# Kernel tuning notes

Hardware: AMD Instinct MI355X
Metric: run time of the kernel (lower is better)

## Reference

```python
import jax, jax.numpy as jnp
import numpy as np

N, K, SD, ID, ZD, ED, H, FC, AT, FT = 10000, 31, 8, 2, 32, 64, 128, 128, 16, 6
DT = 0.25


def setup_inputs() -> dict:
    key = jax.random.key(0)
    ks = iter(jax.random.split(key, 48))

    def p(shape, s=0.08):
        return (s * jax.random.normal(next(ks), shape)).astype(jnp.float32)

    E = N * K
    inp = {
        'state_history': p([4, N, SD], 1.0),          # only last slice is used
        'z': p([N, ZD], 1.0),                         # latent code per node
        'edge_idx1': jnp.repeat(jnp.arange(N), K),    # owning node of each edge
        'edge_idx2': jax.random.randint(next(ks), [E], 0, N),  # neighbor node
        'node_obs_idx': 1 + jnp.arange(E).reshape(N, K),  # +1: row 0 of enc table is the zero-pad row
        'W_edge': p([2 * SD, ED]), 'b_edge': jnp.zeros([ED], jnp.float32),
        'att_W1': p([ED, AT]), 'att_W2': p([SD, AT]), 'att_v': p([AT]),
        'obs_Wi': p([ED, 4 * H]), 'obs_Wh': p([H, 4 * H]), 'obs_b': jnp.zeros([4 * H], jnp.float32),
        'st_Wi': p([SD + ID, 4 * H]), 'st_Wh': p([H, 4 * H]), 'st_b': jnp.zeros([4 * H], jnp.float32),
        'oh0_W': p([SD, H]), 'oh0_b': jnp.zeros([H], jnp.float32),
        'oc0_W': p([SD, H]), 'oc0_b': jnp.zeros([H], jnp.float32),
        'sh0_W': p([SD, H]), 'sh0_b': jnp.zeros([H], jnp.float32),
        'sc0_W': p([SD, H]), 'sc0_b': jnp.zeros([H], jnp.float32),
        'act_W1': p([SD + H + H + ZD, FC]), 'act_b1': jnp.zeros([FC], jnp.float32),
        'act_W2': p([FC, ID]), 'act_b2': jnp.zeros([ID], jnp.float32),
        'dyn_A': p([SD, SD]), 'dyn_B': p([SD, ID]),
        'ft': FT,
    }
    return inp


def _lstm_step(x, h, c, Wi, Wh, b):
    g = x @ Wi + h @ Wh + b
    i, f, gg, o = jnp.split(g, 4, axis=-1)  # torch gate order i,f,g,o
    c2 = jax.nn.sigmoid(f) * c + jax.nn.sigmoid(i) * jnp.tanh(gg)
    h2 = jax.nn.sigmoid(o) * jnp.tanh(c2)
    return h2, c2


def reference(state_history, z, edge_idx1, edge_idx2, node_obs_idx,
              W_edge, b_edge, att_W1, att_W2, att_v,
              obs_Wi, obs_Wh, obs_b, st_Wi, st_Wh, st_b,
              oh0_W, oh0_b, oc0_W, oc0_b, sh0_W, sh0_b, sc0_W, sc0_b,
              act_W1, act_b1, act_W2, act_b2, dyn_A, dyn_B, ft):
    s0 = state_history[-1]                      # [N, SD]
    oh = s0 @ oh0_W + oh0_b                     # LSTM initial states from last history state
    oc = s0 @ oc0_W + oc0_b
    sh = s0 @ sh0_W + sh0_b
    sc = s0 @ sc0_W + sc0_b
    u0 = jnp.zeros((s0.shape[0], dyn_B.shape[1]), s0.dtype)

    def step(carry, _):
        s, u, oh, oc, sh, sc = carry
        # heterogeneous edge encoding: gather endpoint states, encode
        e = jnp.concatenate([s[edge_idx1], s[edge_idx2]], axis=-1)   # [E, 2*SD]
        enc = jax.nn.relu(e @ W_edge + b_edge)                       # [E, ED]
        enc_pad = jnp.concatenate([jnp.zeros((1, enc.shape[1]), enc.dtype), enc], axis=0)
        obs = enc_pad[node_obs_idx]                                  # [N, K, ED] gather
        rel = s - s0                                                  # rel_state_fun
        # additive attention over each node's K observed edges
        score = jnp.einsum('nki,i->nk', jnp.tanh(obs @ att_W1 + (rel @ att_W2)[:, None, :]), att_v)
        alpha = jax.nn.softmax(score, axis=-1)
        ctx = jnp.einsum('nk,nke->ne', alpha, obs)                   # [N, ED]
        oh2, oc2 = _lstm_step(ctx, oh, oc, obs_Wi, obs_Wh, obs_b)
        sh2, sc2 = _lstm_step(jnp.concatenate([rel, u], axis=-1), sh, sc, st_Wi, st_Wh, st_b)
        a = jnp.concatenate([rel, oh2, sh2, z], axis=-1)             # [N, SD+2H+ZD]
        u2 = jax.nn.relu(a @ act_W1 + act_b1) @ act_W2 + act_b2      # action net (input_scale=1)
        s2 = s + DT * (s @ dyn_A.T + u2 @ dyn_B.T)                   # dyn_net rollout
        return (s2, u2, oh2, oc2, sh2, sc2), (s2, u2)

    _, (state_pred, input_pred) = jax.lax.scan(step, (s0, u0, oh, oc, sh, sc), None, length=ft)
    return state_pred, input_pred  # [ft, N, SD], [ft, N, ID]
```

## Files before the change

### kernel.cpp

```cpp
#include <hip/hip_runtime.h>
#include <hip/hip_bf16.h>
#include <math.h>

#define N_NODES 10000
#define KE 31
#define SD 8
#define ID 2
#define ZD 32
#define ED 64
#define HH 128
#define FC 128
#define AT 16
#define FT 6
#define DT_C 0.25f
#define NB 4

#define NTU 32
#define MT 2

#define NKS_O 6
#define NKS_S 5
#define NKS_A 10

#define WP_OBS_SZ 49152
#define WP_ST_SZ  40960
#define WP_ACT_SZ 20480
#define WP_EDGE_SZ 1024
#define WP_ATT1_SZ 512

typedef __bf16 bf16x8 __attribute__((ext_vector_type(8)));
typedef float  f32x4  __attribute__((ext_vector_type(4)));

__device__ __forceinline__ float sigm(float x){ return 1.0f/(1.0f+exp2f(-1.44269504f*x)); }
__device__ __forceinline__ float tanh_f(float x){ return 1.0f - 2.0f/(1.0f+exp2f(2.88539008f*x)); }

__device__ __forceinline__ unsigned short f2b(float f){
  __hip_bfloat16 h = __float2bfloat16(f);
  return __builtin_bit_cast(unsigned short, h);
}
__device__ __forceinline__ float b2f(unsigned short x){
  unsigned int u = ((unsigned int)x) << 16;
  return __builtin_bit_cast(float, u);
}
__device__ __forceinline__ unsigned int pack2(float a, float b){
  return (unsigned int)f2b(a) | ((unsigned int)f2b(b) << 16);
}
__device__ __forceinline__ bf16x8 as_bf16x8(int4 v){
  union { int4 i; bf16x8 b; } u; u.i = v; return u.b;
}
__device__ __forceinline__ int hwaddr(int e, int d){
  return e*64 + ((((d>>3)<<3) ^ ((e&7)<<3)) + (d&7));
}

__global__ __launch_bounds__(256) void pack_weights(
    const float* __restrict__ obs_Wi, const float* __restrict__ obs_Wh,
    const float* __restrict__ st_Wi,  const float* __restrict__ st_Wh,
    const float* __restrict__ act_W1, const float* __restrict__ W_edge,
    const float* __restrict__ att_W1,
    unsigned int* __restrict__ wp_obs, unsigned int* __restrict__ wp_st,
    unsigned int* __restrict__ wp_act, unsigned int* __restrict__ wp_edge,
    unsigned int* __restrict__ wp_att1)
{
  int t = blockIdx.x*256 + threadIdx.x;
  if (t < 49152){
    int c = t / 1536; int r = t - c*1536;
    int ks = r >> 8; int q = r & 255;
    int ln = q >> 2; int dw = q & 3;
    int k  = ks*32 + ((ln>>4)<<3) + dw*2;
    int col = (c<<4) + (ln & 15);
    float v0 = (k   < 64) ? obs_Wi[k*4*HH + col]      : obs_Wh[(k-64)*4*HH + col];
    float v1 = (k+1 < 64) ? obs_Wi[(k+1)*4*HH + col]  : obs_Wh[(k-63)*4*HH + col];
    wp_obs[t] = pack2(v0, v1);
  } else if (t < 90112){
    int t2 = t - 49152;
    int c = t2 / 1280; int r = t2 - c*1280;
    int ks = r >> 8; int q = r & 255;
    int ln = q >> 2; int dw = q & 3;
    int k  = ks*32 + ((ln>>4)<<3) + dw*2;
    int col = (c<<4) + (ln & 15);
    float v0, v1;
    { int kk=k;   v0 = (kk<10)? st_Wi[kk*4*HH+col] : (kk<138 ? st_Wh[(kk-10)*4*HH+col] : 0.f); }
    { int kk=k+1; v1 = (kk<10)? st_Wi[kk*4*HH+col] : (kk<138 ? st_Wh[(kk-10)*4*HH+col] : 0.f); }
    wp_st[t2] = pack2(v0, v1);
  } else if (t < 110592){
    int t3 = t - 90112;
    int c = t3 / 2560; int r = t3 - c*2560;
    int ks = r >> 8; int q = r & 255;
    int ln = q >> 2; int dw = q & 3;
    int k  = ks*32 + ((ln>>4)<<3) + dw*2;
    int col = (c<<4) + (ln & 15);
    float v0 = (k   < 296) ? act_W1[k*FC + col]     : 0.f;
    float v1 = (k+1 < 296) ? act_W1[(k+1)*FC + col] : 0.f;
    wp_act[t3] = pack2(v0, v1);
  } else if (t < 111616){
    int t4 = t - 110592;
    int c = t4 >> 8; int r = t4 & 255;
    int ln = r >> 2; int dw = r & 3;
    int k  = ((ln>>4)<<3) + dw*2;
    int col = (c<<4) + (ln & 15);
    float v0 = (k   < 16) ? W_edge[k*ED + col]     : 0.f;
    float v1 = (k+1 < 16) ? W_edge[(k+1)*ED + col] : 0.f;
    wp_edge[t4] = pack2(v0, v1);
  } else if (t < 112128){
    int t5 = t - 111616;
    int ks = t5 >> 8; int r = t5 & 255;
    int ln = r >> 2; int dw = r & 3;
    int k  = ks*32 + ((ln>>4)<<3) + dw*2;
    int col = ln & 15;
    float v0 = (k   < 64) ? att_W1[k*AT + col]     : 0.f;
    float v1 = (k+1 < 64) ? att_W1[(k+1)*AT + col] : 0.f;
    wp_att1[t5] = pack2(v0, v1);
  }
}

__global__ __launch_bounds__(256) void init_kernel(
    const float* __restrict__ s0,
    const float* __restrict__ oh0_W, const float* __restrict__ oh0_b,
    const float* __restrict__ oc0_W, const float* __restrict__ oc0_b,
    const float* __restrict__ sh0_W, const float* __restrict__ sh0_b,
    const float* __restrict__ sc0_W, const float* __restrict__ sc0_b,
    unsigned short* __restrict__ oh, unsigned short* __restrict__ oc,
    unsigned short* __restrict__ sh, unsigned short* __restrict__ sc,
    float* __restrict__ u, unsigned short* __restrict__ s0bf)
{
  int t = blockIdx.x*256 + threadIdx.x;
  if (t < N_NODES*ID) u[t] = 0.0f;
  if (t < N_NODES*SD) s0bf[t] = f2b(s0[t]);
  if (t >= N_NODES*HH) return;
  int n = t >> 7, j = t & 127;
  float s[SD];
  #pragma unroll
  for (int i=0;i<SD;i++) s[i] = s0[n*SD+i];
  float a0=oh0_b[j], a1=oc0_b[j], a2=sh0_b[j], a3=sc0_b[j];
  #pragma unroll
  for (int i=0;i<SD;i++){
    a0 = fmaf(s[i], oh0_W[i*HH+j], a0);
    a1 = fmaf(s[i], oc0_W[i*HH+j], a1);
    a2 = fmaf(s[i], sh0_W[i*HH+j], a2);
    a3 = fmaf(s[i], sc0_W[i*HH+j], a3);
  }
  oh[t]=f2b(a0); oc[t]=f2b(a1); sh[t]=f2b(a2); sc[t]=f2b(a3);
}

__global__ __launch_bounds__(256) void edge_att_mfma(
    const float* __restrict__ s_prev, const float* __restrict__ s0,
    const unsigned short* __restrict__ sprev_bf,
    const int* __restrict__ edge_idx1, const int* __restrict__ edge_idx2,
    const int* __restrict__ node_obs_idx,
    const unsigned int* __restrict__ wp_edge, const unsigned int* __restrict__ wp_att1,
    const float* __restrict__ b_edge, const float* __restrict__ att_W2,
    const float* __restrict__ att_v, unsigned short* __restrict__ ctx)
{
  __shared__ __align__(16) unsigned int eF[8*64*4];
  __shared__ __align__(16) unsigned short encL[128*64];
  __shared__ __align__(16) unsigned int pF[4*64*4];
  __shared__ float scores[128];
  __shared__ float relbuf[NB][SD];
  __shared__ float relW2b[NB][AT];
  __shared__ unsigned char emask[128];

  const int tid  = threadIdx.x;
  const int lane = tid & 63;
  const int w    = tid >> 6;
  const int n0   = blockIdx.x * NB;
  const int EPB  = NB*KE;

  {
    ((uint4*)pF)[tid] = (uint4){0,0,0,0};
    int eb  = tid >> 1;
    int khi = tid & 1;
    int valid = 0;
    uint4 d = (uint4){0,0,0,0};
    if (eb < EPB){
      int nl = eb / KE;
      int j  = eb - nl*KE;
      int idx = node_obs_idx[(n0+nl)*KE + j];
      if (idx > 0){
        valid = 1;
        int e = idx - 1;
        int i = khi ? edge_idx2[e] : edge_idx1[e];
        d = *(const uint4*)&sprev_bf[i*SD];
      }
    }
    int mt = eb >> 4;
    int base = ((mt<<6) + (eb&15) + (khi<<4)) << 2;
    ((uint4*)&eF[base])[0] = d;
    int zbase = ((mt<<6) + (eb&15) + ((khi+2)<<4)) << 2;
    ((uint4*)&eF[zbase])[0] = (uint4){0,0,0,0};
    if (khi == 0) emask[eb] = (unsigned char)valid;
    if (tid < NB*SD){
      int m = tid >> 3, i = tid & 7;
      relbuf[m][i] = s_prev[(n0+m)*SD + i] - s0[(n0+m)*SD + i];
    }
  }
  __syncthreads();

  if (tid < NB*AT){
    int m = tid >> 4, a = tid & 15;
    float acc = 0.f;
    #pragma unroll
    for (int i = 0; i < SD; ++i) acc = fmaf(relbuf[m][i], att_W2[i*AT + a], acc);
    relW2b[m][a] = acc;
  }
  {
    const int c = lane & 15, g = lane >> 4;
    #pragma unroll
    for (int q = 0; q < 2; ++q){
      int mt = w*2 + q;
      bf16x8 A = as_bf16x8(*(const int4*)&eF[((mt<<6) + lane) << 2]);
      f32x4 acc[4];
      #pragma unroll
      for (int ct = 0; ct < 4; ++ct){
        bf16x8 B = as_bf16x8(*(const int4*)&wp_edge[((ct<<6) + lane) << 2]);
        acc[ct] = (f32x4){0,0,0,0};
        acc[ct] = __builtin_amdgcn_mfma_f32_16x16x32_bf16(A, B, acc[ct], 0, 0, 0);
      }
      #pragma unroll
      for (int ct = 0; ct < 4; ++ct){
        int d = ct*16 + c;
        float bias = b_edge[d];
        #pragma unroll
        for (int r = 0; r < 4; ++r){
          int eb = mt*16 + g*4 + r;
          float v = acc[ct][r] + bias;
          v = emask[eb] ? fmaxf(v, 0.f) : 0.f;
          encL[hwaddr(eb, d)] = f2b(v);
        }
      }
    }
  }
  __syncthreads();

  {
    const int c = lane & 15, g = lane >> 4;
    const float av = att_v[c];
    #pragma unroll
    for (int q = 0; q < 2; ++q){
      int mt = w*2 + q;
      int row = mt*16 + c;
      f32x4 acc = (f32x4){0,0,0,0};
      #pragma unroll
      for (int ks = 0; ks < 2; ++ks){
        int hw = row*64 + (((ks*4 + g) << 3) ^ ((row&7) << 3));
        bf16x8 A = *(const bf16x8*)&encL[hw];
        bf16x8 B = as_bf16x8(*(const int4*)&wp_att1[((ks<<6) + lane) << 2]);
        acc = __builtin_amdgcn_mfma_f32_16x16x32_bf16(A, B, acc, 0, 0, 0);
      }
      #pragma unroll
      for (int r = 0; r < 4; ++r){
        int eb = mt*16 + g*4 + r;
        int nm = eb / KE; if (nm > NB-1) nm = NB-1;
        float sv = av * tanh_f(acc[r] + relW2b[nm][c]);
        #pragma unroll
        for (int off = 1; off < 16; off <<= 1) sv += __shfl_xor(sv, off);
        if (c == 0 && eb < EPB) scores[eb] = sv;
      }
    }
  }
  __syncthreads();

  {
    int m = w;
    float sc_ = (lane < KE) ? scores[m*KE + lane] : -INFINITY;
    float mx = sc_;
    #pragma unroll
    for (int off = 32; off; off >>= 1) mx = fmaxf(mx, __shfl_xor(mx, off));
    float p = (lane < KE) ? exp2f(1.44269504f*(sc_ - mx)) : 0.f;
    float sm = p;
    #pragma unroll
    for (int off = 32; off; off >>= 1) sm += __shfl_xor(sm, off);
    float alpha = p / sm;
    if (lane < KE){
      int k = m*KE + lane;
      int ks = k >> 5;
      int ln = m | (((k>>3)&3) << 4);
      ((unsigned short*)pF)[((ks<<6) + ln)*8 + (k&7)] = f2b(alpha);
    }
  }
  __syncthreads();

  {
    const int c = lane & 15, g = lane >> 4;
    const int d = w*16 + c;
    f32x4 acc = (f32x4){0,0,0,0};
    #pragma unroll
    for (int ks = 0; ks < 4; ++ks){
      bf16x8 A = as_bf16x8(*(const int4*)&pF[((ks<<6) + lane) << 2]);
      union { unsigned short u[8]; bf16x8 v; } bb;
      #pragma unroll
      for (int j = 0; j < 8; ++j){
        int e = ks*32 + g*8 + j;
        bb.u[j] = encL[hwaddr(e, d)];
      }
      acc = __builtin_amdgcn_mfma_f32_16x16x32_bf16(A, bb.v, acc, 0, 0, 0);
    }
    if (g == 0){
      #pragma unroll
      for (int r = 0; r < 4; ++r){
        ctx[(n0 + r)*ED + d] = f2b(acc[r]);
      }
    }
  }
}

__global__ __launch_bounds__(1024) void node_update_mfma(
    const float* __restrict__ s_prev, const float* __restrict__ s0,
    const float* __restrict__ z, const unsigned short* __restrict__ ctx,
    const unsigned int* __restrict__ wp_obs, const unsigned int* __restrict__ wp_st,
    const unsigned int* __restrict__ wp_act,
    const float* __restrict__ obs_b, const float* __restrict__ st_b,
    const float* __restrict__ act_b1,
    const float* __restrict__ act_W2, const float* __restrict__ act_b2,
    const float* __restrict__ dyn_A, const float* __restrict__ dyn_B,
    unsigned short* __restrict__ oh, unsigned short* __restrict__ oc,
    unsigned short* __restrict__ sh, unsigned short* __restrict__ sc,
    float* __restrict__ u, float* __restrict__ s_next,
    unsigned short* __restrict__ snext_bf,
    float* __restrict__ out_state, float* __restrict__ out_input, int tstep)
{
  __shared__ __align__(16) union UB {
    struct { unsigned int X1[MT*NKS_O*64*4]; unsigned int X2[MT*NKS_S*64*4]; } x;
    float F[32][FC+4];
  } ubuf;
  __shared__ __align__(16) unsigned int fragX3[MT*NKS_A*64*4];
  __shared__ float sps[32][SD];
  __shared__ float u2p[32][ID][4];
  __shared__ float u2s[32][ID];

  const int tid  = threadIdx.x;
  const int n0   = blockIdx.x * NTU;
  const int nreal= (N_NODES - n0 < NTU) ? (N_NODES - n0) : NTU;
  const int w    = tid >> 6;
  const int ct   = w & 7;
  const int Mth  = w >> 3;
  const int lane = tid & 63;
  const int hcol = ct*16 + (lane & 15);

  float ocv[4], scv[4];
  #pragma unroll
  for (int r = 0; r < 4; ++r){
    int m = Mth*16 + ((lane>>4)<<2) + r;
    int gn = n0 + m;
    ocv[r] = (m < nreal) ? b2f(oc[gn*HH + hcol]) : 0.f;
    scv[r] = (m < nreal) ? b2f(sc[gn*HH + hcol]) : 0.f;
  }

  for (int idx = tid; idx < 32*96; idx += 1024){
    int m = idx / 96, kp = idx - m*96; int k0 = kp*2; int gn = n0 + m;
    unsigned int d = 0;
    if (m < nreal){
      if (k0 < ED) d = *(const unsigned int*)&ctx[gn*ED + k0];
      else         d = *(const unsigned int*)&oh[gn*HH + k0 - ED];
    }
    int Mt = m >> 4;
    int ln = (m & 15) | (((k0>>3)&3)<<4);
    ubuf.x.X1[(((Mt*NKS_O + (k0>>5))*64 + ln)<<2) + ((k0&7)>>1)] = d;
  }
  for (int idx = tid; idx < 32*80; idx += 1024){
    int m = idx / 80, kp = idx - m*80; int k0 = kp*2; int gn = n0 + m;
    unsigned int d = 0;
    if (m < nreal){
      if (k0 < 8)        d = pack2(s_prev[gn*SD+k0]-s0[gn*SD+k0], s_prev[gn*SD+k0+1]-s0[gn*SD+k0+1]);
      else if (k0 == 8)  d = pack2(u[gn*ID], u[gn*ID+1]);
      else if (k0 < 138) d = *(const unsigned int*)&sh[gn*HH + k0 - 10];
    }
    int Mt = m >> 4;
    int ln = (m & 15) | (((k0>>3)&3)<<4);
    ubuf.x.X2[(((Mt*NKS_S + (k0>>5))*64 + ln)<<2) + ((k0&7)>>1)] = d;
  }
  for (int idx = tid; idx < 32*32; idx += 1024){
    int m = idx / 32, p = idx - m*32; int gn = n0 + m;
    int k0 = (p < 4) ? p*2 : 256 + p*2;
    float v0 = 0.f, v1 = 0.f;
    if (m < nreal){
      if (k0 < 8){ v0 = s_prev[gn*SD+k0]-s0[gn*SD+k0]; v1 = s_prev[gn*SD+k0+1]-s0[gn*SD+k0+1]; }
      else if (k0 < 296){ v0 = z[gn*ZD + k0-264]; v1 = z[gn*ZD + k0-263]; }
    }
    int Mt = m >> 4;
    int ln = (m & 15) | (((k0>>3)&3)<<4);
    fragX3[(((Mt*NKS_A + (k0>>5))*64 + ln)<<2) + ((k0&7)>>1)] = pack2(v0, v1);
  }
  if (tid < NTU*SD){
    int m = tid >> 3, i = tid & 7;
    sps[m][i] = (m < nreal) ? s_prev[(n0+m)*SD + i] : 0.f;
  }
  __syncthreads();

  {
    f32x4 acc[4];
    #pragma unroll
    for (int g = 0; g < 4; ++g){
      float b = obs_b[g*HH + hcol];
      acc[g] = (f32x4){b, b, b, b};
    }
    #pragma unroll
    for (int ks = 0; ks < NKS_O; ++ks){
      bf16x8 a = as_bf16x8(*(const int4*)&ubuf.x.X1[(((Mth*NKS_O + ks)*64 + lane)<<2)]);
      #pragma unroll
      for (int g = 0; g < 4; ++g){
        int c = ct + 8*g;
        bf16x8 b = as_bf16x8(*(const int4*)&wp_obs[(((c*NKS_O + ks)*64 + lane)<<2)]);
        acc[g] = __builtin_amdgcn_mfma_f32_16x16x32_bf16(a, b, acc[g], 0, 0, 0);
      }
    }
    #pragma unroll
    for (int r = 0; r < 4; ++r){
      int m = Mth*16 + ((lane>>4)<<2) + r; int gn = n0 + m;
      float h2 = 0.f;
      if (m < nreal){
        float gi = acc[0][r], gf = acc[1][r], gg = acc[2][r], go = acc[3][r];
        float c2 = sigm(gf)*ocv[r] + sigm(gi)*tanh_f(gg);
        h2 = sigm(go)*tanh_f(c2);
        oc[gn*HH + hcol] = f2b(c2);
        oh[gn*HH + hcol] = f2b(h2);
      }
      int k = 8 + hcol;
      int ln = (m & 15) | (((k>>3)&3)<<4);
      ((unsigned short*)fragX3)[(((m>>4)*NKS_A + (k>>5))*64 + ln)*8 + (k&7)] = f2b(h2);
    }
  }

  {
    f32x4 acc[4];
    #pragma unroll
    for (int g = 0; g < 4; ++g){
      float b = st_b[g*HH + hcol];
      acc[g] = (f32x4){b, b, b, b};
    }
    #pragma unroll
    for (int ks = 0; ks < NKS_S; ++ks){
      bf16x8 a = as_bf16x8(*(const int4*)&ubuf.x.X2[(((Mth*NKS_S + ks)*64 + lane)<<2)]);
      #pragma unroll
      for (int g = 0; g < 4; ++g){
        int c = ct + 8*g;
        bf16x8 b = as_bf16x8(*(const int4*)&wp_st[(((c*NKS_S + ks)*64 + lane)<<2)]);
        acc[g] = __builtin_amdgcn_mfma_f32_16x16x32_bf16(a, b, acc[g], 0, 0, 0);
      }
    }
    #pragma unroll
    for (int r = 0; r < 4; ++r){
      int m = Mth*16 + ((lane>>4)<<2) + r; int gn = n0 + m;
      float h2 = 0.f;
      if (m < nreal){
        float gi = acc[0][r], gf = acc[1][r], gg = acc[2][r], go = acc[3][r];
        float c2 = sigm(gf)*scv[r] + sigm(gi)*tanh_f(gg);
        h2 = sigm(go)*tanh_f(c2);
        sc[gn*HH + hcol] = f2b(c2);
        sh[gn*HH + hcol] = f2b(h2);
      }
      int k = 136 + hcol;
      int ln = (m & 15) | (((k>>3)&3)<<4);
      ((unsigned short*)fragX3)[(((m>>4)*NKS_A + (k>>5))*64 + ln)*8 + (k&7)] = f2b(h2);
    }
  }
  __syncthreads();

  {
    float b1 = act_b1[hcol];
    f32x4 acc = (f32x4){b1, b1, b1, b1};
    #pragma unroll
    for (int ks = 0; ks < NKS_A; ++ks){
      bf16x8 bb = as_bf16x8(*(const int4*)&wp_act[(((ct*NKS_A + ks)*64 + lane)<<2)]);
      bf16x8 a = as_bf16x8(*(const int4*)&fragX3[(((Mth*NKS_A + ks)*64 + lane)<<2)]);
      acc = __builtin_amdgcn_mfma_f32_16x16x32_bf16(a, bb, acc, 0, 0, 0);
    }
    #pragma unroll
    for (int r = 0; r < 4; ++r){
      int m = Mth*16 + ((lane>>4)<<2) + r;
      ubuf.F[m][hcol] = fmaxf(acc[r], 0.f);
    }
  }
  __syncthreads();

  if (tid < 32*ID*4){
    int m  = tid >> 3;
    int c  = (tid >> 2) & 1;
    int kq = tid & 3;
    float p = 0.f;
    #pragma unroll
    for (int i = 0; i < 32; ++i){
      int j = kq*32 + i;
      p = fmaf(ubuf.F[m][j], act_W2[j*ID + c], p);
    }
    u2p[m][c][kq] = p;
  }
  __syncthreads();
  if (tid < NTU*ID){
    int m = tid >> 1, c = tid & 1; int gn = n0 + m;
    if (m < nreal){
      float s = act_b2[c] + u2p[m][c][0] + u2p[m][c][1] + u2p[m][c][2] + u2p[m][c][3];
      u2s[m][c] = s;
      u[gn*ID + c] = s;
      out_input[tstep*N_NODES*ID + gn*ID + c] = s;
    }
  }
  __syncthreads();

  if (tid < NTU*SD){
    int m = tid >> 3, d = tid & 7; int gn = n0 + m;
    if (m < nreal){
      float acc = 0.f;
      #pragma unroll
      for (int e = 0; e < SD; ++e) acc = fmaf(sps[m][e], dyn_A[d*SD+e], acc);
      #pragma unroll
      for (int c = 0; c < ID; ++c) acc = fmaf(u2s[m][c], dyn_B[d*ID+c], acc);
      float s2v = sps[m][d] + DT_C*acc;
      s_next[gn*SD+d] = s2v;
      snext_bf[gn*SD+d] = f2b(s2v);
      out_state[tstep*N_NODES*SD + gn*SD + d] = s2v;
    }
  }
}

extern "C" void kernel_launch(void* const* d_in, const int* in_sizes, int n_in,
                              void* d_out, int out_size, void* d_ws, size_t ws_size,
                              hipStream_t stream)
{
  const float* state_history = (const float*)d_in[0];
  const float* z        = (const float*)d_in[1];
  const int*   edge_idx1 = (const int*)d_in[2];
  const int*   edge_idx2 = (const int*)d_in[3];
  const int*   node_obs_idx = (const int*)d_in[4];
  const float* W_edge  = (const float*)d_in[5];
  const float* b_edge  = (const float*)d_in[6];
  const float* att_W1  = (const float*)d_in[7];
  const float* att_W2  = (const float*)d_in[8];
  const float* att_v   = (const float*)d_in[9];
  const float* obs_Wi  = (const float*)d_in[10];
  const float* obs_Wh  = (const float*)d_in[11];
  const float* obs_b   = (const float*)d_in[12];
  const float* st_Wi   = (const float*)d_in[13];
  const float* st_Wh   = (const float*)d_in[14];
  const float* st_b    = (const float*)d_in[15];
  const float* oh0_W   = (const float*)d_in[16];
  const float* oh0_b   = (const float*)d_in[17];
  const float* oc0_W   = (const float*)d_in[18];
  const float* oc0_b   = (const float*)d_in[19];
  const float* sh0_W   = (const float*)d_in[20];
  const float* sh0_b   = (const float*)d_in[21];
  const float* sc0_W   = (const float*)d_in[22];
  const float* sc0_b   = (const float*)d_in[23];
  const float* act_W1  = (const float*)d_in[24];
  const float* act_b1  = (const float*)d_in[25];
  const float* act_W2  = (const float*)d_in[26];
  const float* act_b2  = (const float*)d_in[27];
  const float* dyn_A   = (const float*)d_in[28];
  const float* dyn_B   = (const float*)d_in[29];

  const float* s0 = state_history + 3*N_NODES*SD;

  float* wsf = (float*)d_ws;
  float* sbuf0 = wsf;
  float* sbuf1 = sbuf0 + N_NODES*SD;
  float* u     = sbuf1 + N_NODES*SD;
  unsigned short* oh    = (unsigned short*)(u + N_NODES*ID);
  unsigned short* oc    = oh + N_NODES*HH;
  unsigned short* sh    = oc + N_NODES*HH;
  unsigned short* sc    = sh + N_NODES*HH;
  unsigned short* ctx   = sc + N_NODES*HH;
  unsigned short* s0bf  = ctx + N_NODES*ED;
  unsigned short* sbf0  = s0bf + N_NODES*SD;
  unsigned short* sbf1  = sbf0 + N_NODES*SD;
  float* sbuf[2] = { sbuf0, sbuf1 };
  unsigned short* sbf[2] = { sbf0, sbf1 };

  unsigned int* wp_obs  = (unsigned int*)(sbf1 + N_NODES*SD);
  unsigned int* wp_st   = wp_obs + WP_OBS_SZ;
  unsigned int* wp_act  = wp_st  + WP_ST_SZ;
  unsigned int* wp_edge = wp_act + WP_ACT_SZ;
  unsigned int* wp_att1 = wp_edge + WP_EDGE_SZ;

  float* out_state = (float*)d_out;
  float* out_input = out_state + FT*N_NODES*SD;

  hipLaunchKernelGGL(pack_weights, dim3(438), dim3(256), 0, stream,
      obs_Wi, obs_Wh, st_Wi, st_Wh, act_W1, W_edge, att_W1,
      wp_obs, wp_st, wp_act, wp_edge, wp_att1);

  hipLaunchKernelGGL(init_kernel, dim3((N_NODES*HH+255)/256), dim3(256), 0, stream,
      s0, oh0_W, oh0_b, oc0_W, oc0_b, sh0_W, sh0_b, sc0_W, sc0_b, oh, oc, sh, sc, u, s0bf);

  const int grid2 = (N_NODES + NTU - 1) / NTU;
  for (int t = 0; t < FT; ++t){
    const float* s_prev = (t==0) ? s0 : sbuf[(t-1)&1];
    const unsigned short* sprev_bf = (t==0) ? s0bf : sbf[(t-1)&1];
    float* s_next = sbuf[t&1];
    unsigned short* snext_bf = sbf[t&1];
    hipLaunchKernelGGL(edge_att_mfma, dim3(N_NODES/NB), dim3(256), 0, stream,
        s_prev, s0, sprev_bf, edge_idx1, edge_idx2, node_obs_idx,
        wp_edge, wp_att1, b_edge, att_W2, att_v, ctx);
    hipLaunchKernelGGL(node_update_mfma, dim3(grid2), dim3(1024), 0, stream,
        s_prev, s0, z, ctx,
        wp_obs, wp_st, wp_act,
        obs_b, st_b, act_b1, act_W2, act_b2, dyn_A, dyn_B,
        oh, oc, sh, sc, u, s_next, snext_bf, out_state, out_input, t);
  }
}
```

Baseline: 358.9 us.

## Retile node update to 40 nodes per block with 12 waves each doing two tiles

Moves the node update kernel from 32 nodes per block on 1024 threads to 40 nodes per block on 768 threads. The 40 nodes are padded to three 16-row M tiles, so there are 24 tile units (3 M tiles times 8 column tiles) and each of the 12 waves handles two of them. Because 10000 divides evenly by 40, the partial-block guards are removed. The intent is fewer blocks, fewer threads per block and better wave packing, at the cost of wasted MFMA work on the 8 padded rows of the third M tile.

```diff
diff --git a/kernel.cpp b/kernel.cpp
--- a/kernel.cpp
+++ b/kernel.cpp
@@ -15,8 +15,9 @@
 #define DT_C 0.25f
 #define NB 4
 
-#define NTU 32
-#define MT 2
+#define NTU 40
+#define MT 3
+#define NWV 12
 
 #define NKS_O 6
 #define NKS_S 5
@@ -303,7 +304,7 @@
   }
 }
 
-__global__ __launch_bounds__(1024) void node_update_mfma(
+__global__ __launch_bounds__(768) void node_update_mfma(
     const float* __restrict__ s_prev, const float* __restrict__ s0,
     const float* __restrict__ z, const unsigned short* __restrict__ ctx,
     const unsigned int* __restrict__ wp_obs, const unsigned int* __restrict__ wp_st,
@@ -320,35 +321,37 @@
 {
   __shared__ __align__(16) union UB {
     struct { unsigned int X1[MT*NKS_O*64*4]; unsigned int X2[MT*NKS_S*64*4]; } x;
-    float F[32][FC+4];
+    float F[48][FC+4];
   } ubuf;
   __shared__ __align__(16) unsigned int fragX3[MT*NKS_A*64*4];
-  __shared__ float sps[32][SD];
-  __shared__ float u2p[32][ID][4];
-  __shared__ float u2s[32][ID];
+  __shared__ float sps[48][SD];
+  __shared__ float u2p[48][ID][4];
+  __shared__ float u2s[48][ID];
 
   const int tid  = threadIdx.x;
   const int n0   = blockIdx.x * NTU;
-  const int nreal= (N_NODES - n0 < NTU) ? (N_NODES - n0) : NTU;
   const int w    = tid >> 6;
-  const int ct   = w & 7;
-  const int Mth  = w >> 3;
   const int lane = tid & 63;
-  const int hcol = ct*16 + (lane & 15);
-
-  float ocv[4], scv[4];
+
+  float ocv[2][4], scv[2][4];
   #pragma unroll
-  for (int r = 0; r < 4; ++r){
-    int m = Mth*16 + ((lane>>4)<<2) + r;
-    int gn = n0 + m;
-    ocv[r] = (m < nreal) ? b2f(oc[gn*HH + hcol]) : 0.f;
-    scv[r] = (m < nreal) ? b2f(sc[gn*HH + hcol]) : 0.f;
-  }
-
-  for (int idx = tid; idx < 32*96; idx += 1024){
+  for (int s = 0; s < 2; ++s){
+    int uq = w + NWV*s;
+    int Mt = uq >> 3, ct = uq & 7;
+    int hc = ct*16 + (lane & 15);
+    #pragma unroll
+    for (int r = 0; r < 4; ++r){
+      int m = Mt*16 + ((lane>>4)<<2) + r;
+      int gn = n0 + m;
+      ocv[s][r] = (m < NTU) ? b2f(oc[gn*HH + hc]) : 0.f;
+      scv[s][r] = (m < NTU) ? b2f(sc[gn*HH + hc]) : 0.f;
+    }
+  }
+
+  for (int idx = tid; idx < 48*96; idx += 768){
     int m = idx / 96, kp = idx - m*96; int k0 = kp*2; int gn = n0 + m;
     unsigned int d = 0;
-    if (m < nreal){
+    if (m < NTU){
       if (k0 < ED) d = *(const unsigned int*)&ctx[gn*ED + k0];
       else         d = *(const unsigned int*)&oh[gn*HH + k0 - ED];
     }
@@ -356,10 +359,10 @@
     int ln = (m & 15) | (((k0>>3)&3)<<4);
     ubuf.x.X1[(((Mt*NKS_O + (k0>>5))*64 + ln)<<2) + ((k0&7)>>1)] = d;
   }
-  for (int idx = tid; idx < 32*80; idx += 1024){
+  for (int idx = tid; idx < 48*80; idx += 768){
     int m = idx / 80, kp = idx - m*80; int k0 = kp*2; int gn = n0 + m;
     unsigned int d = 0;
-    if (m < nreal){
+    if (m < NTU){
       if (k0 < 8)        d = pack2(s_prev[gn*SD+k0]-s0[gn*SD+k0], s_prev[gn*SD+k0+1]-s0[gn*SD+k0+1]);
       else if (k0 == 8)  d = pack2(u[gn*ID], u[gn*ID+1]);
       else if (k0 < 138) d = *(const unsigned int*)&sh[gn*HH + k0 - 10];
@@ -368,11 +371,11 @@
     int ln = (m & 15) | (((k0>>3)&3)<<4);
     ubuf.x.X2[(((Mt*NKS_S + (k0>>5))*64 + ln)<<2) + ((k0&7)>>1)] = d;
   }
-  for (int idx = tid; idx < 32*32; idx += 1024){
+  for (int idx = tid; idx < 48*32; idx += 768){
     int m = idx / 32, p = idx - m*32; int gn = n0 + m;
     int k0 = (p < 4) ? p*2 : 256 + p*2;
     float v0 = 0.f, v1 = 0.f;
-    if (m < nreal){
+    if (m < NTU){
       if (k0 < 8){ v0 = s_prev[gn*SD+k0]-s0[gn*SD+k0]; v1 = s_prev[gn*SD+k0+1]-s0[gn*SD+k0+1]; }
       else if (k0 < 296){ v0 = z[gn*ZD + k0-264]; v1 = z[gn*ZD + k0-263]; }
     }
@@ -382,20 +385,24 @@
   }
   if (tid < NTU*SD){
     int m = tid >> 3, i = tid & 7;
-    sps[m][i] = (m < nreal) ? s_prev[(n0+m)*SD + i] : 0.f;
-  }
-  __syncthreads();
-
-  {
+    sps[m][i] = s_prev[(n0+m)*SD + i];
+  }
+  __syncthreads();
+
+  #pragma unroll
+  for (int s = 0; s < 2; ++s){
+    int uq = w + NWV*s;
+    int Mt = uq >> 3, ct = uq & 7;
+    int hc = ct*16 + (lane & 15);
     f32x4 acc[4];
     #pragma unroll
     for (int g = 0; g < 4; ++g){
-      float b = obs_b[g*HH + hcol];
+      float b = obs_b[g*HH + hc];
       acc[g] = (f32x4){b, b, b, b};
     }
     #pragma unroll
     for (int ks = 0; ks < NKS_O; ++ks){
-      bf16x8 a = as_bf16x8(*(const int4*)&ubuf.x.X1[(((Mth*NKS_O + ks)*64 + lane)<<2)]);
+      bf16x8 a = as_bf16x8(*(const int4*)&ubuf.x.X1[(((Mt*NKS_O + ks)*64 + lane)<<2)]);
       #pragma unroll
       for (int g = 0; g < 4; ++g){
         int c = ct + 8*g;
@@ -405,31 +412,35 @@
     }
     #pragma unroll
     for (int r = 0; r < 4; ++r){
-      int m = Mth*16 + ((lane>>4)<<2) + r; int gn = n0 + m;
+      int m = Mt*16 + ((lane>>4)<<2) + r; int gn = n0 + m;
       float h2 = 0.f;
-      if (m < nreal){
+      if (m < NTU){
         float gi = acc[0][r], gf = acc[1][r], gg = acc[2][r], go = acc[3][r];
-        float c2 = sigm(gf)*ocv[r] + sigm(gi)*tanh_f(gg);
+        float c2 = sigm(gf)*ocv[s][r] + sigm(gi)*tanh_f(gg);
         h2 = sigm(go)*tanh_f(c2);
-        oc[gn*HH + hcol] = f2b(c2);
-        oh[gn*HH + hcol] = f2b(h2);
-      }
-      int k = 8 + hcol;
+        oc[gn*HH + hc] = f2b(c2);
+        oh[gn*HH + hc] = f2b(h2);
+      }
+      int k = 8 + hc;
       int ln = (m & 15) | (((k>>3)&3)<<4);
       ((unsigned short*)fragX3)[(((m>>4)*NKS_A + (k>>5))*64 + ln)*8 + (k&7)] = f2b(h2);
     }
   }
 
-  {
+  #pragma unroll
+  for (int s = 0; s < 2; ++s){
+    int uq = w + NWV*s;
+    int Mt = uq >> 3, ct = uq & 7;
+    int hc = ct*16 + (lane & 15);
     f32x4 acc[4];
     #pragma unroll
     for (int g = 0; g < 4; ++g){
-      float b = st_b[g*HH + hcol];
+      float b = st_b[g*HH + hc];
       acc[g] = (f32x4){b, b, b, b};
     }
     #pragma unroll
     for (int ks = 0; ks < NKS_S; ++ks){
-      bf16x8 a = as_bf16x8(*(const int4*)&ubuf.x.X2[(((Mth*NKS_S + ks)*64 + lane)<<2)]);
+      bf16x8 a = as_bf16x8(*(const int4*)&ubuf.x.X2[(((Mt*NKS_S + ks)*64 + lane)<<2)]);
       #pragma unroll
       for (int g = 0; g < 4; ++g){
         int c = ct + 8*g;
@@ -439,40 +450,44 @@
     }
     #pragma unroll
     for (int r = 0; r < 4; ++r){
-      int m = Mth*16 + ((lane>>4)<<2) + r; int gn = n0 + m;
+      int m = Mt*16 + ((lane>>4)<<2) + r; int gn = n0 + m;
       float h2 = 0.f;
-      if (m < nreal){
+      if (m < NTU){
         float gi = acc[0][r], gf = acc[1][r], gg = acc[2][r], go = acc[3][r];
-        float c2 = sigm(gf)*scv[r] + sigm(gi)*tanh_f(gg);
+        float c2 = sigm(gf)*scv[s][r] + sigm(gi)*tanh_f(gg);
         h2 = sigm(go)*tanh_f(c2);
-        sc[gn*HH + hcol] = f2b(c2);
-        sh[gn*HH + hcol] = f2b(h2);
-      }
-      int k = 136 + hcol;
+        sc[gn*HH + hc] = f2b(c2);
+        sh[gn*HH + hc] = f2b(h2);
+      }
+      int k = 136 + hc;
       int ln = (m & 15) | (((k>>3)&3)<<4);
       ((unsigned short*)fragX3)[(((m>>4)*NKS_A + (k>>5))*64 + ln)*8 + (k&7)] = f2b(h2);
     }
   }
   __syncthreads();
 
-  {
-    float b1 = act_b1[hcol];
+  #pragma unroll
+  for (int s = 0; s < 2; ++s){
+    int uq = w + NWV*s;
+    int Mt = uq >> 3, ct = uq & 7;
+    int hc = ct*16 + (lane & 15);
+    float b1 = act_b1[hc];
     f32x4 acc = (f32x4){b1, b1, b1, b1};
     #pragma unroll
     for (int ks = 0; ks < NKS_A; ++ks){
       bf16x8 bb = as_bf16x8(*(const int4*)&wp_act[(((ct*NKS_A + ks)*64 + lane)<<2)]);
-      bf16x8 a = as_bf16x8(*(const int4*)&fragX3[(((Mth*NKS_A + ks)*64 + lane)<<2)]);
+      bf16x8 a = as_bf16x8(*(const int4*)&fragX3[(((Mt*NKS_A + ks)*64 + lane)<<2)]);
       acc = __builtin_amdgcn_mfma_f32_16x16x32_bf16(a, bb, acc, 0, 0, 0);
     }
     #pragma unroll
     for (int r = 0; r < 4; ++r){
-      int m = Mth*16 + ((lane>>4)<<2) + r;
-      ubuf.F[m][hcol] = fmaxf(acc[r], 0.f);
-    }
-  }
-  __syncthreads();
-
-  if (tid < 32*ID*4){
+      int m = Mt*16 + ((lane>>4)<<2) + r;
+      ubuf.F[m][hc] = fmaxf(acc[r], 0.f);
+    }
+  }
+  __syncthreads();
+
+  if (tid < 48*ID*4){
     int m  = tid >> 3;
     int c  = (tid >> 2) & 1;
     int kq = tid & 3;
@@ -487,28 +502,24 @@
   __syncthreads();
   if (tid < NTU*ID){
     int m = tid >> 1, c = tid & 1; int gn = n0 + m;
-    if (m < nreal){
-      float s = act_b2[c] + u2p[m][c][0] + u2p[m][c][1] + u2p[m][c][2] + u2p[m][c][3];
-      u2s[m][c] = s;
-      u[gn*ID + c] = s;
-      out_input[tstep*N_NODES*ID + gn*ID + c] = s;
-    }
+    float s = act_b2[c] + u2p[m][c][0] + u2p[m][c][1] + u2p[m][c][2] + u2p[m][c][3];
+    u2s[m][c] = s;
+    u[gn*ID + c] = s;
+    out_input[tstep*N_NODES*ID + gn*ID + c] = s;
   }
   __syncthreads();
 
   if (tid < NTU*SD){
     int m = tid >> 3, d = tid & 7; int gn = n0 + m;
-    if (m < nreal){
-      float acc = 0.f;
-      #pragma unroll
-      for (int e = 0; e < SD; ++e) acc = fmaf(sps[m][e], dyn_A[d*SD+e], acc);
-      #pragma unroll
-      for (int c = 0; c < ID; ++c) acc = fmaf(u2s[m][c], dyn_B[d*ID+c], acc);
-      float s2v = sps[m][d] + DT_C*acc;
-      s_next[gn*SD+d] = s2v;
-      snext_bf[gn*SD+d] = f2b(s2v);
-      out_state[tstep*N_NODES*SD + gn*SD + d] = s2v;
-    }
+    float acc = 0.f;
+    #pragma unroll
+    for (int e = 0; e < SD; ++e) acc = fmaf(sps[m][e], dyn_A[d*SD+e], acc);
+    #pragma unroll
+    for (int c = 0; c < ID; ++c) acc = fmaf(u2s[m][c], dyn_B[d*ID+c], acc);
+    float s2v = sps[m][d] + DT_C*acc;
+    s_next[gn*SD+d] = s2v;
+    snext_bf[gn*SD+d] = f2b(s2v);
+    out_state[tstep*N_NODES*SD + gn*SD + d] = s2v;
   }
 }
 
@@ -580,7 +591,6 @@
   hipLaunchKernelGGL(init_kernel, dim3((N_NODES*HH+255)/256), dim3(256), 0, stream,
       s0, oh0_W, oh0_b, oc0_W, oc0_b, sh0_W, sh0_b, sc0_W, sc0_b, oh, oc, sh, sc, u, s0bf);
 
-  const int grid2 = (N_NODES + NTU - 1) / NTU;
   for (int t = 0; t < FT; ++t){
     const float* s_prev = (t==0) ? s0 : sbuf[(t-1)&1];
     const unsigned short* sprev_bf = (t==0) ? s0bf : sbf[(t-1)&1];
@@ -589,7 +599,7 @@
     hipLaunchKernelGGL(edge_att_mfma, dim3(N_NODES/NB), dim3(256), 0, stream,
         s_prev, s0, sprev_bf, edge_idx1, edge_idx2, node_obs_idx,
         wp_edge, wp_att1, b_edge, att_W2, att_v, ctx);
-    hipLaunchKernelGGL(node_update_mfma, dim3(grid2), dim3(1024), 0, stream,
+    hipLaunchKernelGGL(node_update_mfma, dim3(N_NODES/NTU), dim3(768), 0, stream,
         s_prev, s0, z, ctx,
         wp_obs, wp_st, wp_act,
         obs_b, st_b, act_b1, act_W2, act_b2, dyn_A, dyn_B,
```

New measurement: 306.9 us. -14.5%, faster.
